# Kernel tuning notes

Hardware: AMD Instinct MI355X
Metric: run time of the kernel (lower is better)

The kernel has to match this reference:

```python
import jax, jax.numpy as jnp
import numpy as np

N_HIGH = 4096
N_LOW = 262144
E_HIGH = 65536
E_LOW = 524288
IN_DIM = 128
OUT_DIM = 128
HEADS = 4
HEAD_DIM = OUT_DIM // HEADS
EPS = 1e-5
SCALE = np.float32(1.0 / np.sqrt(HEAD_DIM))


def _layernorm(x, w, b):
    m = jnp.mean(x, axis=-1, keepdims=True)
    v = jnp.var(x, axis=-1, keepdims=True)
    return (x - m) * jax.lax.rsqrt(v + EPS) * w + b


def _transformer_conv(x, edge_index, Wq, bq, Wk, bk, Wv, bv, Wskip, bskip, num_nodes):
    # PyG TransformerConv: q from target node, k/v from source node, per-head
    # softmax over incoming edges, concat heads, plus skip connection.
    q = (x @ Wq + bq).reshape(num_nodes, HEADS, HEAD_DIM)
    k = (x @ Wk + bk).reshape(num_nodes, HEADS, HEAD_DIM)
    v = (x @ Wv + bv).reshape(num_nodes, HEADS, HEAD_DIM)
    src, dst = edge_index[0], edge_index[1]
    score = jnp.einsum('ehd,ehd->eh', q[dst], k[src]) * SCALE  # [E, H]
    m = jax.ops.segment_max(score, dst, num_segments=num_nodes)
    e = jnp.exp(score - m[dst])
    denom = jax.ops.segment_sum(e, dst, num_segments=num_nodes)
    alpha = e / denom[dst]
    agg = jax.ops.segment_sum(alpha[:, :, None] * v[src], dst, num_segments=num_nodes)
    return agg.reshape(num_nodes, OUT_DIM) + x @ Wskip + bskip


def setup_inputs() -> dict:
    key = jax.random.key(0)
    ks = jax.random.split(key, 12)
    sw = np.float32(1.0 / np.sqrt(IN_DIM))
    sa = np.float32(1.0 / np.sqrt(2 * OUT_DIM))
    return {
        'high_emb': jax.random.normal(ks[0], (N_HIGH, IN_DIM), jnp.float32),
        'low_emb': jax.random.normal(ks[1], (N_LOW, IN_DIM), jnp.float32),
        'Wq': jax.random.normal(ks[2], (IN_DIM, OUT_DIM), jnp.float32) * sw,
        'bq': jnp.zeros((OUT_DIM,), jnp.float32),
        'Wk': jax.random.normal(ks[3], (IN_DIM, OUT_DIM), jnp.float32) * sw,
        'bk': jnp.zeros((OUT_DIM,), jnp.float32),
        'Wv': jax.random.normal(ks[4], (IN_DIM, OUT_DIM), jnp.float32) * sw,
        'bv': jnp.zeros((OUT_DIM,), jnp.float32),
        'Wskip': jax.random.normal(ks[5], (IN_DIM, OUT_DIM), jnp.float32) * sw,
        'bskip': jnp.zeros((OUT_DIM,), jnp.float32),
        'ln_w': jnp.ones((OUT_DIM,), jnp.float32),
        'ln_b': jnp.zeros((OUT_DIM,), jnp.float32),
        'w_lh': jax.random.normal(ks[6], (2 * OUT_DIM, 1), jnp.float32) * sa,
        'w_hl': jax.random.normal(ks[7], (2 * OUT_DIM, 1), jnp.float32) * sa,
        'edge_index_high': jax.random.randint(ks[8], (2, E_HIGH), 0, N_HIGH, jnp.int32),
        'edge_index_low': jax.random.randint(ks[9], (2, E_LOW), 0, N_LOW, jnp.int32),
        'batch': jnp.sort(jax.random.randint(ks[10], (N_LOW,), 0, N_HIGH, jnp.int32)),
    }


def reference(high_emb, low_emb, Wq, bq, Wk, bk, Wv, bv, Wskip, bskip, ln_w, ln_b, w_lh, w_hl, edge_index_high, edge_index_low, batch):
    h = _transformer_conv(high_emb, edge_index_high, Wq, bq, Wk, bk, Wv, bv, Wskip, bskip, N_HIGH)
    l = _transformer_conv(low_emb, edge_index_low, Wq, bq, Wk, bk, Wv, bv, Wskip, bskip, N_LOW)
    h = jax.nn.relu(_layernorm(h, ln_w, ln_b))
    l = jax.nn.relu(_layernorm(l, ln_w, ln_b))
    # global_mean_pool over low nodes per graph
    counts = jax.ops.segment_sum(jnp.ones((N_LOW,), jnp.float32), batch, num_segments=N_HIGH)
    pooled = jax.ops.segment_sum(l, batch, num_segments=N_HIGH) / jnp.maximum(counts, 1.0)[:, None]
    sim = jax.nn.sigmoid(jnp.concatenate([h, pooled], axis=1) @ w_lh)  # [N_HIGH, 1]
    high_out = sim * h + (1.0 - sim) * pooled
    # vectorized form of the per-graph loop: broadcast high node to its low nodes
    hb = h[batch]  # [N_LOW, OUT_DIM]
    a = jax.nn.sigmoid(jnp.concatenate([hb, l], axis=1) @ w_hl)  # [N_LOW, 1]
    low_out = a * l + (1.0 - a) * hb
    return (high_out, low_out)
```

## Files before the change

kernel.cpp:

```cpp
#include <hip/hip_runtime.h>
#include <hip/hip_bf16.h>
#include <math.h>

#define N_HIGH 4096
#define N_LOW 262144
#define E_HIGH 65536
#define E_LOW 524288
#define LN_EPS 1e-5f
#define ATT_SCALE 0.17677669529663687f

typedef short bf16x8 __attribute__((ext_vector_type(8)));
typedef float f32x4 __attribute__((ext_vector_type(4)));

__device__ __forceinline__ float bf2f(unsigned int u) {
    union { unsigned int i; float f; } v; v.i = u << 16; return v.f;
}
__device__ __forceinline__ unsigned short f2bf(float f) {
    union { unsigned int i; float f; } v; v.f = f;
    unsigned int r = (v.i + 0x7fffu + ((v.i >> 16) & 1u)) >> 16;
    return (unsigned short)r;
}
__device__ __forceinline__ float ldf(const void* p, size_t i, int isbf) {
    if (isbf) return bf2f(((const unsigned short*)p)[i]);
    return ((const float*)p)[i];
}
__device__ __forceinline__ float4 load4f(const void* p, size_t i, int isbf) {
    if (isbf) {
        uint2 u = *(const uint2*)((const unsigned short*)p + i);
        float4 r;
        r.x = bf2f(u.x & 0xffffu); r.y = bf2f(u.x >> 16);
        r.z = bf2f(u.y & 0xffffu); r.w = bf2f(u.y >> 16);
        return r;
    }
    return *(const float4*)((const float*)p + i);
}
__device__ __forceinline__ void stf(void* p, size_t i, float v, int isbf) {
    if (isbf) ((unsigned short*)p)[i] = f2bf(v);
    else      ((float*)p)[i] = v;
}
__device__ __forceinline__ void unpack8(uint4 u, float* f) {
    f[0] = bf2f(u.x & 0xffffu); f[1] = bf2f(u.x >> 16);
    f[2] = bf2f(u.y & 0xffffu); f[3] = bf2f(u.y >> 16);
    f[4] = bf2f(u.z & 0xffffu); f[5] = bf2f(u.z >> 16);
    f[6] = bf2f(u.w & 0xffffu); f[7] = bf2f(u.w >> 16);
}
__device__ __forceinline__ uint4 pack8(const float* f) {
    uint4 u;
    u.x = (unsigned)f2bf(f[0]) | ((unsigned)f2bf(f[1]) << 16);
    u.y = (unsigned)f2bf(f[2]) | ((unsigned)f2bf(f[3]) << 16);
    u.z = (unsigned)f2bf(f[4]) | ((unsigned)f2bf(f[5]) << 16);
    u.w = (unsigned)f2bf(f[6]) | ((unsigned)f2bf(f[7]) << 16);
    return u;
}

__global__ __launch_bounds__(256) void probe_dtype_kernel(
    const unsigned int* __restrict__ x, int* __restrict__ flag)
{
    __shared__ int cnt;
    if (threadIdx.x == 0) cnt = 0;
    __syncthreads();
    unsigned int b = (x[threadIdx.x] >> 8) & 0x7fu;
    if (b >= 60u && b <= 65u) atomicAdd(&cnt, 1);
    __syncthreads();
    if (threadIdx.x == 0) *flag = (cnt >= 128) ? 1 : 0;
}

__global__ __launch_bounds__(256) void prep_wt_kernel(
    const void* __restrict__ Wq, const void* __restrict__ Wk,
    const void* __restrict__ Wv, const void* __restrict__ Ws,
    const void* __restrict__ lnw, const void* __restrict__ lnb,
    const void* __restrict__ whl,
    unsigned short* __restrict__ Wt, float* __restrict__ lnwbf,
    float* __restrict__ whlf, const int* __restrict__ dflag)
{
    const int isbf = *dflag;
    if (blockIdx.x >= 32) {
        int t = threadIdx.x;
        lnwbf[t] = (t < 128) ? ldf(lnw, t, isbf) : ldf(lnb, t - 128, isbf);
        whlf[t] = ldf(whl, t, isbf);
        return;
    }
    const int g = blockIdx.x >> 3;
    const int slice = blockIdx.x & 7;
    const void* W = (g == 0) ? Wq : (g == 1) ? Wk : (g == 2) ? Wv : Ws;
    #pragma unroll
    for (int i = 0; i < 8; ++i) {
        int linear = i * 256 + threadIdx.x;
        int k = slice * 16 + (linear >> 7);
        int n = linear & 127;
        float v = ldf(W, (size_t)k * 128 + n, isbf);
        Wt[((size_t)g * 128 + n) * 128 + k] = f2bf(v);
    }
}

__global__ __launch_bounds__(256) void gemm_mfma_kernel(
    const void* __restrict__ x, const unsigned short* __restrict__ Wt,
    const void* __restrict__ bq, const void* __restrict__ bk,
    const void* __restrict__ bv, const void* __restrict__ bs,
    unsigned short* __restrict__ qkv, unsigned short* __restrict__ accv,
    const int* __restrict__ dflag)
{
    __shared__ unsigned short As[64 * 136];
    __shared__ unsigned short Bs[128 * 136];
    const int isbf = *dflag;
    const int tid = threadIdx.x;
    const int m0 = blockIdx.x * 64;

    #pragma unroll
    for (int i = 0; i < 8; ++i) {
        int linear = i * 256 + tid;
        int row = linear >> 5;
        int c4 = (linear & 31) << 2;
        float4 v = load4f(x, (size_t)(m0 + row) * 128 + c4, isbf);
        ushort4 s;
        s.x = f2bf(v.x); s.y = f2bf(v.y); s.z = f2bf(v.z); s.w = f2bf(v.w);
        *(ushort4*)&As[row * 136 + c4] = s;
    }

    const void* blist[4] = { bq, bk, bv, bs };

    const int lane = tid & 63;
    const int w = tid >> 6;
    const int wm = (w & 1) * 32;
    const int wn = (w >> 1) * 64;
    const int lr = lane & 15;
    const int lk = (lane >> 4) * 8;
    const int rbase = (lane >> 4) * 4;

    for (int c = 0; c < 4; ++c) {
        __syncthreads();
        #pragma unroll
        for (int i = 0; i < 8; ++i) {
            int linear = i * 256 + tid;
            int n = linear >> 4;
            int c8 = (linear & 15) << 3;
            uint4 v = *(const uint4*)&Wt[((size_t)c * 128 + n) * 128 + c8];
            *(uint4*)&Bs[n * 136 + c8] = v;
        }
        __syncthreads();

        f32x4 acc[2][4];
        #pragma unroll
        for (int a = 0; a < 2; ++a)
            #pragma unroll
            for (int b = 0; b < 4; ++b) acc[a][b] = (f32x4){0.f, 0.f, 0.f, 0.f};

        #pragma unroll
        for (int kk = 0; kk < 4; ++kk) {
            int k0 = kk * 32 + lk;
            bf16x8 af[2], bfv[4];
            #pragma unroll
            for (int im = 0; im < 2; ++im)
                af[im] = *(const bf16x8*)&As[(wm + im * 16 + lr) * 136 + k0];
            #pragma unroll
            for (int in = 0; in < 4; ++in)
                bfv[in] = *(const bf16x8*)&Bs[(wn + in * 16 + lr) * 136 + k0];
            #pragma unroll
            for (int im = 0; im < 2; ++im)
                #pragma unroll
                for (int in = 0; in < 4; ++in)
                    acc[im][in] = __builtin_amdgcn_mfma_f32_16x16x32_bf16(
                        af[im], bfv[in], acc[im][in], 0, 0, 0);
        }

        float bias[4];
        #pragma unroll
        for (int in = 0; in < 4; ++in) bias[in] = ldf(blist[c], wn + in * 16 + lr, isbf);

        #pragma unroll
        for (int im = 0; im < 2; ++im) {
            #pragma unroll
            for (int r = 0; r < 4; ++r) {
                int m = wm + im * 16 + rbase + r;
                size_t row = (size_t)(m0 + m);
                #pragma unroll
                for (int in = 0; in < 4; ++in) {
                    int n = wn + in * 16 + lr;
                    float val = acc[im][in][r] + bias[in];
                    if (c < 3) qkv[row * 384 + c * 128 + n] = f2bf(val);
                    else       accv[row * 128 + n] = f2bf(val);
                }
            }
        }
    }
}

__global__ __launch_bounds__(256) void count_deg_kernel(
    const int* __restrict__ ei, int E, int* __restrict__ deg)
{
    int e = blockIdx.x * 256 + threadIdx.x;
    if (e >= E) return;
    atomicAdd(&deg[ei[E + e]], 1);
}

__global__ __launch_bounds__(256) void scan1_kernel(
    const int* __restrict__ deg, int* __restrict__ pre, int* __restrict__ bsum)
{
    __shared__ int wsum[4];
    int tid = threadIdx.x;
    int lane = tid & 63, w = tid >> 6;
    int base = blockIdx.x * 1024 + tid * 4;
    int4 v = *(const int4*)(deg + base);
    int s = v.x + v.y + v.z + v.w;
    int inc = s;
    #pragma unroll
    for (int m = 1; m < 64; m <<= 1) {
        int t = __shfl_up(inc, m, 64);
        if (lane >= m) inc += t;
    }
    if (lane == 63) wsum[w] = inc;
    __syncthreads();
    int woff = 0;
    #pragma unroll
    for (int j = 0; j < 4; ++j) if (j < w) woff += wsum[j];
    int excl = woff + inc - s;
    pre[base]     = excl;
    pre[base + 1] = excl + v.x;
    pre[base + 2] = excl + v.x + v.y;
    pre[base + 3] = excl + v.x + v.y + v.z;
    if (tid == 0) bsum[blockIdx.x] = wsum[0] + wsum[1] + wsum[2] + wsum[3];
}

__global__ void scan2_kernel(int* __restrict__ bsum, int NB)
{
    if (threadIdx.x == 0 && blockIdx.x == 0) {
        int run = 0;
        for (int i = 0; i < NB; ++i) { int t = bsum[i]; bsum[i] = run; run += t; }
    }
}

__global__ __launch_bounds__(256) void scan3_kernel(
    const int* __restrict__ pre, const int* __restrict__ bsum,
    int* __restrict__ off, int N)
{
    int i = blockIdx.x * 256 + threadIdx.x;
    if (i >= N) return;
    off[i] = pre[i] + bsum[i >> 10];
}

__global__ __launch_bounds__(256) void fill_csr_kernel(
    const int* __restrict__ ei, int E, int* __restrict__ off,
    int* __restrict__ csr)
{
    int e = blockIdx.x * 256 + threadIdx.x;
    if (e >= E) return;
    int dst = ei[E + e];
    int pos = atomicAdd(&off[dst], 1);
    csr[pos] = ei[e];
}

__global__ __launch_bounds__(256) void attn_gather_ln_kernel(
    const unsigned short* __restrict__ qkv, const int* __restrict__ csr_src,
    const int* __restrict__ off_end, const int* __restrict__ deg,
    unsigned short* skip_out, const float* __restrict__ lnwbf, int N)
{
    int il = threadIdx.x & 15;
    int n = blockIdx.x * 16 + (threadIdx.x >> 4);
    if (n >= N) return;
    int end = off_end[n];
    int cnt = deg[n];
    int p = end - cnt;

    float qf[8];
    unpack8(*(const uint4*)(qkv + (long)n * 384 + 8 * il), qf);
    float acc[8] = {0.f, 0.f, 0.f, 0.f, 0.f, 0.f, 0.f, 0.f};
    float den = 0.f;

    int it = 0;
    for (; it + 1 < cnt; it += 2) {
        int s0 = csr_src[p + it];
        int s1 = csr_src[p + it + 1];
        const unsigned short* b0 = qkv + (long)s0 * 384 + 8 * il;
        const unsigned short* b1 = qkv + (long)s1 * 384 + 8 * il;
        uint4 k0w = *(const uint4*)(b0 + 128);
        uint4 v0w = *(const uint4*)(b0 + 256);
        uint4 k1w = *(const uint4*)(b1 + 128);
        uint4 v1w = *(const uint4*)(b1 + 256);
        float kf[8], vf[8], kg[8], vg[8];
        unpack8(k0w, kf); unpack8(v0w, vf);
        unpack8(k1w, kg); unpack8(v1w, vg);
        float p0 = 0.f, p1 = 0.f;
        #pragma unroll
        for (int j = 0; j < 8; ++j) { p0 += qf[j] * kf[j]; p1 += qf[j] * kg[j]; }
        p0 += __shfl_xor(p0, 1, 64); p1 += __shfl_xor(p1, 1, 64);
        p0 += __shfl_xor(p0, 2, 64); p1 += __shfl_xor(p1, 2, 64);
        float e0 = __expf(fminf(fmaxf(p0 * ATT_SCALE, -60.f), 60.f));
        float e1 = __expf(fminf(fmaxf(p1 * ATT_SCALE, -60.f), 60.f));
        den += e0 + e1;
        #pragma unroll
        for (int j = 0; j < 8; ++j) acc[j] += e0 * vf[j] + e1 * vg[j];
    }
    if (it < cnt) {
        int s0 = csr_src[p + it];
        const unsigned short* b0 = qkv + (long)s0 * 384 + 8 * il;
        uint4 k0w = *(const uint4*)(b0 + 128);
        uint4 v0w = *(const uint4*)(b0 + 256);
        float kf[8], vf[8];
        unpack8(k0w, kf); unpack8(v0w, vf);
        float p0 = 0.f;
        #pragma unroll
        for (int j = 0; j < 8; ++j) p0 += qf[j] * kf[j];
        p0 += __shfl_xor(p0, 1, 64);
        p0 += __shfl_xor(p0, 2, 64);
        float e0 = __expf(fminf(fmaxf(p0 * ATT_SCALE, -60.f), 60.f));
        den += e0;
        #pragma unroll
        for (int j = 0; j < 8; ++j) acc[j] += e0 * vf[j];
    }

    float inv = (cnt > 0) ? 1.f / den : 0.f;
    float x[8];
    unpack8(*(const uint4*)(skip_out + (long)n * 128 + 8 * il), x);
    float s = 0.f, qq = 0.f;
    #pragma unroll
    for (int j = 0; j < 8; ++j) {
        x[j] = acc[j] * inv + x[j];
        s += x[j];
        qq += x[j] * x[j];
    }
    #pragma unroll
    for (int m = 1; m < 16; m <<= 1) {
        s += __shfl_xor(s, m, 64);
        qq += __shfl_xor(qq, m, 64);
    }
    float mean = s * (1.f / 128.f);
    float var = fmaxf(qq * (1.f / 128.f) - mean * mean, 0.f);
    float rs = rsqrtf(var + LN_EPS);
    float4 wA = *(const float4*)(lnwbf + 8 * il);
    float4 wB = *(const float4*)(lnwbf + 8 * il + 4);
    float4 bA = *(const float4*)(lnwbf + 128 + 8 * il);
    float4 bB = *(const float4*)(lnwbf + 128 + 8 * il + 4);
    float wv[8] = {wA.x, wA.y, wA.z, wA.w, wB.x, wB.y, wB.z, wB.w};
    float bv[8] = {bA.x, bA.y, bA.z, bA.w, bB.x, bB.y, bB.z, bB.w};
    float y[8];
    #pragma unroll
    for (int j = 0; j < 8; ++j)
        y[j] = fmaxf((x[j] - mean) * rs * wv[j] + bv[j], 0.f);
    *(uint4*)(skip_out + (long)n * 128 + 8 * il) = pack8(y);
}

__global__ __launch_bounds__(128) void pool_kernel(
    const unsigned short* __restrict__ l, const int* __restrict__ batch,
    float* __restrict__ pooled)
{
    __shared__ int se[2];
    int g = blockIdx.x;
    if (threadIdx.x == 0) {
        int lo = 0, hi = N_LOW;
        while (lo < hi) { int mid = (lo + hi) >> 1; if (batch[mid] < g) lo = mid + 1; else hi = mid; }
        se[0] = lo;
        hi = N_LOW;
        while (lo < hi) { int mid = (lo + hi) >> 1; if (batch[mid] < g + 1) lo = mid + 1; else hi = mid; }
        se[1] = lo;
    }
    __syncthreads();
    int start = se[0], end = se[1];
    int d = threadIdx.x;
    float s0 = 0.f, s1 = 0.f, s2 = 0.f, s3 = 0.f;
    int r = start;
    for (; r + 3 < end; r += 4) {
        s0 += bf2f(l[(long)r * 128 + d]);
        s1 += bf2f(l[(long)(r + 1) * 128 + d]);
        s2 += bf2f(l[(long)(r + 2) * 128 + d]);
        s3 += bf2f(l[(long)(r + 3) * 128 + d]);
    }
    for (; r < end; ++r) s0 += bf2f(l[(long)r * 128 + d]);
    int cnt = end - start;
    pooled[(long)g * 128 + d] = ((s0 + s1) + (s2 + s3)) / (float)(cnt > 0 ? cnt : 1);
}

__global__ __launch_bounds__(256) void high_out_kernel(
    const unsigned short* __restrict__ h, const float* __restrict__ pooled,
    const void* __restrict__ wlh, void* __restrict__ out,
    const int* __restrict__ dflag)
{
    const int isbf = *dflag;
    int lane = threadIdx.x & 63;
    int n = blockIdx.x * 4 + (threadIdx.x >> 6);
    if (n >= N_HIGH) return;
    float h0 = bf2f(h[(long)n * 128 + 2 * lane]);
    float h1 = bf2f(h[(long)n * 128 + 2 * lane + 1]);
    float2 pv = *(const float2*)(pooled + (long)n * 128 + 2 * lane);
    float s = h0 * ldf(wlh, 2 * lane, isbf) + h1 * ldf(wlh, 2 * lane + 1, isbf)
            + pv.x * ldf(wlh, 128 + 2 * lane, isbf) + pv.y * ldf(wlh, 128 + 2 * lane + 1, isbf);
    #pragma unroll
    for (int m = 1; m < 64; m <<= 1) s += __shfl_xor(s, m, 64);
    float sim = 1.f / (1.f + __expf(-s));
    stf(out, (size_t)n * 128 + 2 * lane,     sim * h0 + (1.f - sim) * pv.x, isbf);
    stf(out, (size_t)n * 128 + 2 * lane + 1, sim * h1 + (1.f - sim) * pv.y, isbf);
}

__global__ __launch_bounds__(256) void low_out_kernel(
    const unsigned short* __restrict__ l, const unsigned short* __restrict__ h,
    const int* __restrict__ batch, const float* __restrict__ whlf,
    void* __restrict__ out, const int* __restrict__ dflag)
{
    const int isbf = *dflag;
    int il = threadIdx.x & 15;
    int n = blockIdx.x * 16 + (threadIdx.x >> 4);
    if (n >= N_LOW) return;
    int g = batch[n];
    float lf[8], hf[8];
    unpack8(*(const uint4*)(l + (long)n * 128 + 8 * il), lf);
    unpack8(*(const uint4*)(h + (long)g * 128 + 8 * il), hf);
    float4 wh0 = *(const float4*)(whlf + 8 * il);
    float4 wh1 = *(const float4*)(whlf + 8 * il + 4);
    float4 wl0 = *(const float4*)(whlf + 128 + 8 * il);
    float4 wl1 = *(const float4*)(whlf + 128 + 8 * il + 4);
    float s = hf[0] * wh0.x + hf[1] * wh0.y + hf[2] * wh0.z + hf[3] * wh0.w
            + hf[4] * wh1.x + hf[5] * wh1.y + hf[6] * wh1.z + hf[7] * wh1.w
            + lf[0] * wl0.x + lf[1] * wl0.y + lf[2] * wl0.z + lf[3] * wl0.w
            + lf[4] * wl1.x + lf[5] * wl1.y + lf[6] * wl1.z + lf[7] * wl1.w;
    #pragma unroll
    for (int m = 1; m < 16; m <<= 1) s += __shfl_xor(s, m, 64);
    float a = 1.f / (1.f + __expf(-s));
    float y[8];
    #pragma unroll
    for (int j = 0; j < 8; ++j) y[j] = a * lf[j] + (1.f - a) * hf[j];
    size_t base = (size_t)N_HIGH * 128 + (size_t)n * 128 + 8 * il;
    if (isbf) {
        *(uint4*)((unsigned short*)out + base) = pack8(y);
    } else {
        float* o = (float*)out + base;
        *(float4*)o       = (float4){y[0], y[1], y[2], y[3]};
        *(float4*)(o + 4) = (float4){y[4], y[5], y[6], y[7]};
    }
}

extern "C" void kernel_launch(void* const* d_in, const int* in_sizes, int n_in,
                              void* d_out, int out_size, void* d_ws, size_t ws_size,
                              hipStream_t stream)
{
    const void* high_emb = d_in[0];
    const void* low_emb  = d_in[1];
    const void* Wq = d_in[2];  const void* bq = d_in[3];
    const void* Wk = d_in[4];  const void* bk = d_in[5];
    const void* Wv = d_in[6];  const void* bv = d_in[7];
    const void* Ws = d_in[8];  const void* bs = d_in[9];
    const void* ln_w = d_in[10];
    const void* ln_b = d_in[11];
    const void* w_lh = d_in[12];
    const void* w_hl = d_in[13];
    const int* ei_high = (const int*)d_in[14];
    const int* ei_low  = (const int*)d_in[15];
    const int* batch   = (const int*)d_in[16];

    char* ws = (char*)d_ws;
    const size_t OFF_QKV_LOW  = 0;
    const size_t OFF_ACC_LOW  = 201326592;
    const size_t OFF_AUX      = 335544320;
    const size_t OFF_QKV_HIGH = 348127232;
    const size_t OFF_ACC_HIGH = 351272960;
    const size_t OFF_POOLED   = 354484224;
    const size_t OFF_FLAG     = 356581376;
    const size_t WS_NEEDED    = 356581632;
    if (ws_size < WS_NEEDED) return;

    unsigned short* qkv_low  = (unsigned short*)(ws + OFF_QKV_LOW);
    unsigned short* acc_low  = (unsigned short*)(ws + OFF_ACC_LOW);
    unsigned short* qkv_high = (unsigned short*)(ws + OFF_QKV_HIGH);
    unsigned short* acc_high = (unsigned short*)(ws + OFF_ACC_HIGH);
    float*          pooled   = (float*)(ws + OFF_POOLED);
    int*            dflag    = (int*)(ws + OFF_FLAG);

    unsigned short* Wt    = (unsigned short*)(ws + OFF_AUX);
    float* lnwbf = (float*)(ws + OFF_AUX + 131072);
    float* whlf  = (float*)(ws + OFF_AUX + 132096);
    int* deg_low  = (int*)(ws + OFF_AUX +  262144);
    int* pre_low  = (int*)(ws + OFF_AUX + 1310720);
    int* off_low  = (int*)(ws + OFF_AUX + 2359296);
    int* csr_low  = (int*)(ws + OFF_AUX + 3407872);
    int* deg_high = (int*)(ws + OFF_AUX + 5505024);
    int* pre_high = (int*)(ws + OFF_AUX + 5521408);
    int* off_high = (int*)(ws + OFF_AUX + 5537792);
    int* csr_high = (int*)(ws + OFF_AUX + 5554176);
    int* bsum     = (int*)(ws + OFF_AUX + 5816320);

    unsigned short* l_low  = acc_low;
    unsigned short* h_high = acc_high;

    hipMemsetAsync(deg_low, 0, (size_t)N_LOW * sizeof(int), stream);
    hipMemsetAsync(deg_high, 0, (size_t)N_HIGH * sizeof(int), stream);

    probe_dtype_kernel<<<1, 256, 0, stream>>>((const unsigned int*)high_emb, dflag);

    count_deg_kernel<<<E_LOW / 256, 256, 0, stream>>>(ei_low, E_LOW, deg_low);
    count_deg_kernel<<<E_HIGH / 256, 256, 0, stream>>>(ei_high, E_HIGH, deg_high);

    scan1_kernel<<<N_LOW / 1024, 256, 0, stream>>>(deg_low, pre_low, bsum);
    scan2_kernel<<<1, 64, 0, stream>>>(bsum, N_LOW / 1024);
    scan3_kernel<<<N_LOW / 256, 256, 0, stream>>>(pre_low, bsum, off_low, N_LOW);

    scan1_kernel<<<N_HIGH / 1024, 256, 0, stream>>>(deg_high, pre_high, bsum);
    scan2_kernel<<<1, 64, 0, stream>>>(bsum, N_HIGH / 1024);
    scan3_kernel<<<N_HIGH / 256, 256, 0, stream>>>(pre_high, bsum, off_high, N_HIGH);

    fill_csr_kernel<<<E_LOW / 256, 256, 0, stream>>>(ei_low, E_LOW, off_low, csr_low);
    fill_csr_kernel<<<E_HIGH / 256, 256, 0, stream>>>(ei_high, E_HIGH, off_high, csr_high);

    prep_wt_kernel<<<33, 256, 0, stream>>>(Wq, Wk, Wv, Ws, ln_w, ln_b, w_hl,
                                           Wt, lnwbf, whlf, dflag);

    gemm_mfma_kernel<<<N_HIGH / 64, 256, 0, stream>>>(
        high_emb, Wt, bq, bk, bv, bs, qkv_high, acc_high, dflag);
    gemm_mfma_kernel<<<N_LOW / 64, 256, 0, stream>>>(
        low_emb, Wt, bq, bk, bv, bs, qkv_low, acc_low, dflag);

    attn_gather_ln_kernel<<<N_HIGH / 16, 256, 0, stream>>>(
        qkv_high, csr_high, off_high, deg_high, acc_high, lnwbf, N_HIGH);
    attn_gather_ln_kernel<<<N_LOW / 16, 256, 0, stream>>>(
        qkv_low, csr_low, off_low, deg_low, acc_low, lnwbf, N_LOW);

    pool_kernel<<<N_HIGH, 128, 0, stream>>>(l_low, batch, pooled);

    high_out_kernel<<<N_HIGH / 4, 256, 0, stream>>>(h_high, pooled, w_lh, d_out, dflag);
    low_out_kernel<<<N_LOW / 16, 256, 0, stream>>>(l_low, h_high, batch, whlf, d_out, dflag);
}
```

Measured before the change: 615.2 us.

## Make projection GEMM persistent with full weight matrix resident in shared memory

Replaces the per-64-row GEMM, which reloaded each of the four 128x128 weight slices into LDS per block, with a persistent 1024-thread kernel that loads all four weight matrices once into 128KB of XOR-swizzled LDS. Each block then loops over 128-row tiles, reading A fragments straight from global memory and converting them to bf16 in registers. It swaps the MFMA operand order so results can be stored as packed 4-element rows, and precomputes biases as floats in the prep kernel. The cost it targets is the repeated weight staging and the scalar bf16 stores. In exchange it relies on a very large LDS allocation and uncached direct global A loads, each of which is reused across four MFMAs.

```diff
diff --git a/kernel.cpp b/kernel.cpp
--- a/kernel.cpp
+++ b/kernel.cpp
@@ -23,16 +23,6 @@
 __device__ __forceinline__ float ldf(const void* p, size_t i, int isbf) {
     if (isbf) return bf2f(((const unsigned short*)p)[i]);
     return ((const float*)p)[i];
-}
-__device__ __forceinline__ float4 load4f(const void* p, size_t i, int isbf) {
-    if (isbf) {
-        uint2 u = *(const uint2*)((const unsigned short*)p + i);
-        float4 r;
-        r.x = bf2f(u.x & 0xffffu); r.y = bf2f(u.x >> 16);
-        r.z = bf2f(u.y & 0xffffu); r.w = bf2f(u.y >> 16);
-        return r;
-    }
-    return *(const float4*)((const float*)p + i);
 }
 __device__ __forceinline__ void stf(void* p, size_t i, float v, int isbf) {
     if (isbf) ((unsigned short*)p)[i] = f2bf(v);
@@ -68,13 +58,25 @@
 __global__ __launch_bounds__(256) void prep_wt_kernel(
     const void* __restrict__ Wq, const void* __restrict__ Wk,
     const void* __restrict__ Wv, const void* __restrict__ Ws,
+    const void* __restrict__ bq, const void* __restrict__ bk,
+    const void* __restrict__ bv, const void* __restrict__ bs,
     const void* __restrict__ lnw, const void* __restrict__ lnb,
     const void* __restrict__ whl,
     unsigned short* __restrict__ Wt, float* __restrict__ lnwbf,
-    float* __restrict__ whlf, const int* __restrict__ dflag)
+    float* __restrict__ whlf, float* __restrict__ biasf,
+    const int* __restrict__ dflag)
 {
     const int isbf = *dflag;
-    if (blockIdx.x >= 32) {
+    if (blockIdx.x == 33) {
+        const void* bl[4] = { bq, bk, bv, bs };
+        #pragma unroll
+        for (int j = 0; j < 2; ++j) {
+            int idx = j * 256 + threadIdx.x;
+            biasf[idx] = ldf(bl[idx >> 7], idx & 127, isbf);
+        }
+        return;
+    }
+    if (blockIdx.x == 32) {
         int t = threadIdx.x;
         lnwbf[t] = (t < 128) ? ldf(lnw, t, isbf) : ldf(lnb, t - 128, isbf);
         whlf[t] = ldf(whl, t, isbf);
@@ -93,93 +95,97 @@
     }
 }
 
-__global__ __launch_bounds__(256) void gemm_mfma_kernel(
+__global__ __launch_bounds__(1024, 4) void gemm_persist_kernel(
     const void* __restrict__ x, const unsigned short* __restrict__ Wt,
-    const void* __restrict__ bq, const void* __restrict__ bk,
-    const void* __restrict__ bv, const void* __restrict__ bs,
+    const float* __restrict__ biasf,
     unsigned short* __restrict__ qkv, unsigned short* __restrict__ accv,
-    const int* __restrict__ dflag)
-{
-    __shared__ unsigned short As[64 * 136];
-    __shared__ unsigned short Bs[128 * 136];
+    const int* __restrict__ dflag, int ntiles)
+{
+    __shared__ unsigned short Bs[512 * 128];
     const int isbf = *dflag;
     const int tid = threadIdx.x;
-    const int m0 = blockIdx.x * 64;
 
     #pragma unroll
     for (int i = 0; i < 8; ++i) {
-        int linear = i * 256 + tid;
-        int row = linear >> 5;
-        int c4 = (linear & 31) << 2;
-        float4 v = load4f(x, (size_t)(m0 + row) * 128 + c4, isbf);
-        ushort4 s;
-        s.x = f2bf(v.x); s.y = f2bf(v.y); s.z = f2bf(v.z); s.w = f2bf(v.w);
-        *(ushort4*)&As[row * 136 + c4] = s;
-    }
-
-    const void* blist[4] = { bq, bk, bv, bs };
+        int L = i * 1024 + tid;
+        int row = L >> 4;
+        int cp = L & 15;
+        int cl = cp ^ (row & 15);
+        uint4 v = *(const uint4*)&Wt[(row << 7) + (cl << 3)];
+        *(uint4*)&Bs[(row << 7) + (cp << 3)] = v;
+    }
+    __syncthreads();
 
     const int lane = tid & 63;
     const int w = tid >> 6;
-    const int wm = (w & 1) * 32;
-    const int wn = (w >> 1) * 64;
-    const int lr = lane & 15;
-    const int lk = (lane >> 4) * 8;
-    const int rbase = (lane >> 4) * 4;
-
-    for (int c = 0; c < 4; ++c) {
-        __syncthreads();
-        #pragma unroll
-        for (int i = 0; i < 8; ++i) {
-            int linear = i * 256 + tid;
-            int n = linear >> 4;
-            int c8 = (linear & 15) << 3;
-            uint4 v = *(const uint4*)&Wt[((size_t)c * 128 + n) * 128 + c8];
-            *(uint4*)&Bs[n * 136 + c8] = v;
-        }
-        __syncthreads();
-
-        f32x4 acc[2][4];
-        #pragma unroll
-        for (int a = 0; a < 2; ++a)
+    const int lrm = lane & 15;
+    const int q = lane >> 4;
+    const int wm = (w >> 3) << 6;
+    const int wn = (w & 7) << 6;
+    const int c = wn >> 7;
+    const int nb = wn & 127;
+
+    for (int t = blockIdx.x; t < ntiles; t += gridDim.x) {
+        __builtin_amdgcn_s_barrier();
+        const int m0 = t << 7;
+        f32x4 acc[4][4];
+        #pragma unroll
+        for (int a = 0; a < 4; ++a)
             #pragma unroll
             for (int b = 0; b < 4; ++b) acc[a][b] = (f32x4){0.f, 0.f, 0.f, 0.f};
 
-        #pragma unroll
+        const int arow0 = m0 + wm + lrm;
+        #pragma unroll 1
         for (int kk = 0; kk < 4; ++kk) {
-            int k0 = kk * 32 + lk;
-            bf16x8 af[2], bfv[4];
+            bf16x8 bfv[4];
             #pragma unroll
-            for (int im = 0; im < 2; ++im)
-                af[im] = *(const bf16x8*)&As[(wm + im * 16 + lr) * 136 + k0];
+            for (int in = 0; in < 4; ++in) {
+                int brow = wn + (in << 4) + lrm;
+                int cp = ((kk << 2) + q) ^ lrm;
+                bfv[in] = *(const bf16x8*)&Bs[(brow << 7) + (cp << 3)];
+            }
+            const int kcol = (kk << 5) + (q << 3);
             #pragma unroll
-            for (int in = 0; in < 4; ++in)
-                bfv[in] = *(const bf16x8*)&Bs[(wn + in * 16 + lr) * 136 + k0];
-            #pragma unroll
-            for (int im = 0; im < 2; ++im)
+            for (int im = 0; im < 4; ++im) {
+                bf16x8 af;
+                if (isbf) {
+                    af = *(const bf16x8*)((const unsigned short*)x
+                            + (((size_t)(arow0 + (im << 4))) << 7) + kcol);
+                } else {
+                    const float* xf = (const float*)x
+                            + (((size_t)(arow0 + (im << 4))) << 7) + kcol;
+                    float4 lo = *(const float4*)xf;
+                    float4 hi = *(const float4*)(xf + 4);
+                    union { bf16x8 v; unsigned short u[8]; } t8;
+                    t8.u[0] = f2bf(lo.x); t8.u[1] = f2bf(lo.y);
+                    t8.u[2] = f2bf(lo.z); t8.u[3] = f2bf(lo.w);
+                    t8.u[4] = f2bf(hi.x); t8.u[5] = f2bf(hi.y);
+                    t8.u[6] = f2bf(hi.z); t8.u[7] = f2bf(hi.w);
+                    af = t8.v;
+                }
                 #pragma unroll
                 for (int in = 0; in < 4; ++in)
                     acc[im][in] = __builtin_amdgcn_mfma_f32_16x16x32_bf16(
-                        af[im], bfv[in], acc[im][in], 0, 0, 0);
+                        bfv[in], af, acc[im][in], 0, 0, 0);
+            }
         }
 
-        float bias[4];
-        #pragma unroll
-        for (int in = 0; in < 4; ++in) bias[in] = ldf(blist[c], wn + in * 16 + lr, isbf);
-
-        #pragma unroll
-        for (int im = 0; im < 2; ++im) {
+        #pragma unroll
+        for (int im = 0; im < 4; ++im) {
+            int m = m0 + wm + (im << 4) + lrm;
             #pragma unroll
-            for (int r = 0; r < 4; ++r) {
-                int m = wm + im * 16 + rbase + r;
-                size_t row = (size_t)(m0 + m);
-                #pragma unroll
-                for (int in = 0; in < 4; ++in) {
-                    int n = wn + in * 16 + lr;
-                    float val = acc[im][in][r] + bias[in];
-                    if (c < 3) qkv[row * 384 + c * 128 + n] = f2bf(val);
-                    else       accv[row * 128 + n] = f2bf(val);
-                }
+            for (int in = 0; in < 4; ++in) {
+                int n4 = nb + (in << 4) + (q << 2);
+                float4 b4 = *(const float4*)&biasf[(c << 7) + n4];
+                float v0 = acc[im][in][0] + b4.x;
+                float v1 = acc[im][in][1] + b4.y;
+                float v2 = acc[im][in][2] + b4.z;
+                float v3 = acc[im][in][3] + b4.w;
+                uint2 pk;
+                pk.x = (unsigned)f2bf(v0) | ((unsigned)f2bf(v1) << 16);
+                pk.y = (unsigned)f2bf(v2) | ((unsigned)f2bf(v3) << 16);
+                if (c < 3) *(uint2*)&qkv[(size_t)m * 384 + (c << 7) + n4] = pk;
+                else       *(uint2*)&accv[(((size_t)m) << 7) + n4] = pk;
             }
         }
     }
@@ -466,6 +472,7 @@
     unsigned short* Wt    = (unsigned short*)(ws + OFF_AUX);
     float* lnwbf = (float*)(ws + OFF_AUX + 131072);
     float* whlf  = (float*)(ws + OFF_AUX + 132096);
+    float* biasf = (float*)(ws + OFF_AUX + 133120);
     int* deg_low  = (int*)(ws + OFF_AUX +  262144);
     int* pre_low  = (int*)(ws + OFF_AUX + 1310720);
     int* off_low  = (int*)(ws + OFF_AUX + 2359296);
@@ -498,13 +505,14 @@
     fill_csr_kernel<<<E_LOW / 256, 256, 0, stream>>>(ei_low, E_LOW, off_low, csr_low);
     fill_csr_kernel<<<E_HIGH / 256, 256, 0, stream>>>(ei_high, E_HIGH, off_high, csr_high);
 
-    prep_wt_kernel<<<33, 256, 0, stream>>>(Wq, Wk, Wv, Ws, ln_w, ln_b, w_hl,
-                                           Wt, lnwbf, whlf, dflag);
-
-    gemm_mfma_kernel<<<N_HIGH / 64, 256, 0, stream>>>(
-        high_emb, Wt, bq, bk, bv, bs, qkv_high, acc_high, dflag);
-    gemm_mfma_kernel<<<N_LOW / 64, 256, 0, stream>>>(
-        low_emb, Wt, bq, bk, bv, bs, qkv_low, acc_low, dflag);
+    prep_wt_kernel<<<34, 256, 0, stream>>>(Wq, Wk, Wv, Ws, bq, bk, bv, bs,
+                                           ln_w, ln_b, w_hl,
+                                           Wt, lnwbf, whlf, biasf, dflag);
+
+    gemm_persist_kernel<<<N_HIGH / 128, 1024, 0, stream>>>(
+        high_emb, Wt, biasf, qkv_high, acc_high, dflag, N_HIGH / 128);
+    gemm_persist_kernel<<<256, 1024, 0, stream>>>(
+        low_emb, Wt, biasf, qkv_low, acc_low, dflag, N_LOW / 128);
 
     attn_gather_ln_kernel<<<N_HIGH / 16, 256, 0, stream>>>(
         qkv_high, csr_high, off_high, deg_high, acc_high, lnwbf, N_HIGH);
```

Measured after the change: 772.0 us. 25.5% more time.

## Enlarge GEMM tile to 128 rows, swizzle LDS, vectorize transposed epilogue stores

Applied to the files above, without the earlier changes.

The QKV/skip projection GEMM now uses 512-thread blocks covering 128 rows, with XOR-swizzled LDS layouts instead of padded rows. The MFMA operands are swapped so each lane holds four consecutive output columns, which allows packed 8-byte bf16 stores. Biases are pre-converted to float in the prep kernel and read as float4. The goal is fewer weight reloads per row, fewer LDS bank conflicts and more coalesced stores, at the cost of larger shared memory per block and fewer blocks.

```diff
diff --git a/kernel.cpp b/kernel.cpp
--- a/kernel.cpp
+++ b/kernel.cpp
@@ -68,13 +68,25 @@
 __global__ __launch_bounds__(256) void prep_wt_kernel(
     const void* __restrict__ Wq, const void* __restrict__ Wk,
     const void* __restrict__ Wv, const void* __restrict__ Ws,
+    const void* __restrict__ bq, const void* __restrict__ bk,
+    const void* __restrict__ bv, const void* __restrict__ bs,
     const void* __restrict__ lnw, const void* __restrict__ lnb,
     const void* __restrict__ whl,
     unsigned short* __restrict__ Wt, float* __restrict__ lnwbf,
-    float* __restrict__ whlf, const int* __restrict__ dflag)
+    float* __restrict__ whlf, float* __restrict__ biasf,
+    const int* __restrict__ dflag)
 {
     const int isbf = *dflag;
-    if (blockIdx.x >= 32) {
+    if (blockIdx.x == 33) {
+        const void* bl[4] = { bq, bk, bv, bs };
+        #pragma unroll
+        for (int j = 0; j < 2; ++j) {
+            int idx = j * 256 + threadIdx.x;
+            biasf[idx] = ldf(bl[idx >> 7], idx & 127, isbf);
+        }
+        return;
+    }
+    if (blockIdx.x == 32) {
         int t = threadIdx.x;
         lnwbf[t] = (t < 128) ? ldf(lnw, t, isbf) : ldf(lnb, t - 128, isbf);
         whlf[t] = ldf(whl, t, isbf);
@@ -93,49 +105,46 @@
     }
 }
 
-__global__ __launch_bounds__(256) void gemm_mfma_kernel(
+__global__ __launch_bounds__(512, 4) void gemm_mfma_kernel(
     const void* __restrict__ x, const unsigned short* __restrict__ Wt,
-    const void* __restrict__ bq, const void* __restrict__ bk,
-    const void* __restrict__ bv, const void* __restrict__ bs,
+    const float* __restrict__ biasf,
     unsigned short* __restrict__ qkv, unsigned short* __restrict__ accv,
     const int* __restrict__ dflag)
 {
-    __shared__ unsigned short As[64 * 136];
-    __shared__ unsigned short Bs[128 * 136];
+    __shared__ unsigned short As[128 * 128];
+    __shared__ unsigned short Bs[128 * 128];
     const int isbf = *dflag;
     const int tid = threadIdx.x;
-    const int m0 = blockIdx.x * 64;
+    const int m0 = blockIdx.x * 128;
 
     #pragma unroll
     for (int i = 0; i < 8; ++i) {
-        int linear = i * 256 + tid;
+        int linear = i * 512 + tid;
         int row = linear >> 5;
         int c4 = (linear & 31) << 2;
         float4 v = load4f(x, (size_t)(m0 + row) * 128 + c4, isbf);
         ushort4 s;
         s.x = f2bf(v.x); s.y = f2bf(v.y); s.z = f2bf(v.z); s.w = f2bf(v.w);
-        *(ushort4*)&As[row * 136 + c4] = s;
-    }
-
-    const void* blist[4] = { bq, bk, bv, bs };
+        int cl = c4 >> 3, o = c4 & 7;
+        *(ushort4*)&As[(row << 7) + ((cl ^ (row & 15)) << 3) + o] = s;
+    }
 
     const int lane = tid & 63;
     const int w = tid >> 6;
-    const int wm = (w & 1) * 32;
-    const int wn = (w >> 1) * 64;
-    const int lr = lane & 15;
-    const int lk = (lane >> 4) * 8;
-    const int rbase = (lane >> 4) * 4;
+    const int wm = (w & 3) << 5;
+    const int wn = (w >> 2) << 6;
+    const int lrm = lane & 15;
+    const int q = lane >> 4;
 
     for (int c = 0; c < 4; ++c) {
         __syncthreads();
         #pragma unroll
-        for (int i = 0; i < 8; ++i) {
-            int linear = i * 256 + tid;
+        for (int i = 0; i < 4; ++i) {
+            int linear = i * 512 + tid;
             int n = linear >> 4;
-            int c8 = (linear & 15) << 3;
-            uint4 v = *(const uint4*)&Wt[((size_t)c * 128 + n) * 128 + c8];
-            *(uint4*)&Bs[n * 136 + c8] = v;
+            int cl = linear & 15;
+            uint4 v = *(const uint4*)&Wt[((size_t)c * 128 + n) * 128 + (cl << 3)];
+            *(uint4*)&Bs[(n << 7) + ((cl ^ (n & 15)) << 3)] = v;
         }
         __syncthreads();
 
@@ -147,39 +156,38 @@
 
         #pragma unroll
         for (int kk = 0; kk < 4; ++kk) {
-            int k0 = kk * 32 + lk;
+            const int cc = ((kk << 2) + q) ^ lrm;
             bf16x8 af[2], bfv[4];
             #pragma unroll
             for (int im = 0; im < 2; ++im)
-                af[im] = *(const bf16x8*)&As[(wm + im * 16 + lr) * 136 + k0];
+                af[im] = *(const bf16x8*)&As[((wm + (im << 4) + lrm) << 7) + (cc << 3)];
             #pragma unroll
             for (int in = 0; in < 4; ++in)
-                bfv[in] = *(const bf16x8*)&Bs[(wn + in * 16 + lr) * 136 + k0];
+                bfv[in] = *(const bf16x8*)&Bs[((wn + (in << 4) + lrm) << 7) + (cc << 3)];
             #pragma unroll
             for (int im = 0; im < 2; ++im)
                 #pragma unroll
                 for (int in = 0; in < 4; ++in)
                     acc[im][in] = __builtin_amdgcn_mfma_f32_16x16x32_bf16(
-                        af[im], bfv[in], acc[im][in], 0, 0, 0);
+                        bfv[in], af[im], acc[im][in], 0, 0, 0);
         }
 
-        float bias[4];
-        #pragma unroll
-        for (int in = 0; in < 4; ++in) bias[in] = ldf(blist[c], wn + in * 16 + lr, isbf);
-
         #pragma unroll
         for (int im = 0; im < 2; ++im) {
+            int m = m0 + wm + (im << 4) + lrm;
             #pragma unroll
-            for (int r = 0; r < 4; ++r) {
-                int m = wm + im * 16 + rbase + r;
-                size_t row = (size_t)(m0 + m);
-                #pragma unroll
-                for (int in = 0; in < 4; ++in) {
-                    int n = wn + in * 16 + lr;
-                    float val = acc[im][in][r] + bias[in];
-                    if (c < 3) qkv[row * 384 + c * 128 + n] = f2bf(val);
-                    else       accv[row * 128 + n] = f2bf(val);
-                }
+            for (int in = 0; in < 4; ++in) {
+                int n4 = wn + (in << 4) + (q << 2);
+                float4 b4 = *(const float4*)&biasf[(c << 7) + n4];
+                float v0 = acc[im][in][0] + b4.x;
+                float v1 = acc[im][in][1] + b4.y;
+                float v2 = acc[im][in][2] + b4.z;
+                float v3 = acc[im][in][3] + b4.w;
+                uint2 pk;
+                pk.x = (unsigned)f2bf(v0) | ((unsigned)f2bf(v1) << 16);
+                pk.y = (unsigned)f2bf(v2) | ((unsigned)f2bf(v3) << 16);
+                if (c < 3) *(uint2*)&qkv[(size_t)m * 384 + (c << 7) + n4] = pk;
+                else       *(uint2*)&accv[(((size_t)m) << 7) + n4] = pk;
             }
         }
     }
@@ -466,6 +474,7 @@
     unsigned short* Wt    = (unsigned short*)(ws + OFF_AUX);
     float* lnwbf = (float*)(ws + OFF_AUX + 131072);
     float* whlf  = (float*)(ws + OFF_AUX + 132096);
+    float* biasf = (float*)(ws + OFF_AUX + 133120);
     int* deg_low  = (int*)(ws + OFF_AUX +  262144);
     int* pre_low  = (int*)(ws + OFF_AUX + 1310720);
     int* off_low  = (int*)(ws + OFF_AUX + 2359296);
@@ -498,13 +507,14 @@
     fill_csr_kernel<<<E_LOW / 256, 256, 0, stream>>>(ei_low, E_LOW, off_low, csr_low);
     fill_csr_kernel<<<E_HIGH / 256, 256, 0, stream>>>(ei_high, E_HIGH, off_high, csr_high);
 
-    prep_wt_kernel<<<33, 256, 0, stream>>>(Wq, Wk, Wv, Ws, ln_w, ln_b, w_hl,
-                                           Wt, lnwbf, whlf, dflag);
-
-    gemm_mfma_kernel<<<N_HIGH / 64, 256, 0, stream>>>(
-        high_emb, Wt, bq, bk, bv, bs, qkv_high, acc_high, dflag);
-    gemm_mfma_kernel<<<N_LOW / 64, 256, 0, stream>>>(
-        low_emb, Wt, bq, bk, bv, bs, qkv_low, acc_low, dflag);
+    prep_wt_kernel<<<34, 256, 0, stream>>>(Wq, Wk, Wv, Ws, bq, bk, bv, bs,
+                                           ln_w, ln_b, w_hl,
+                                           Wt, lnwbf, whlf, biasf, dflag);
+
+    gemm_mfma_kernel<<<N_HIGH / 128, 512, 0, stream>>>(
+        high_emb, Wt, biasf, qkv_high, acc_high, dflag);
+    gemm_mfma_kernel<<<N_LOW / 128, 512, 0, stream>>>(
+        low_emb, Wt, biasf, qkv_low, acc_low, dflag);
 
     attn_gather_ln_kernel<<<N_HIGH / 16, 256, 0, stream>>>(
         qkv_high, csr_high, off_high, deg_high, acc_high, lnwbf, N_HIGH);
```

Measured after the change: 621.1 us. No clear change (+1.0%).
